# Optimization experiments

Measured on AMD Instinct MI355X. Metric: run time of the kernel, lower is better.

The kernel has to match this reference:

```python
import jax, jax.numpy as jnp
import numpy as np

D_MODEL = 1024
D_STATE = 16
D_CONV = 4
EXPAND = 2
D_INNER = EXPAND * D_MODEL          # 2048
DT_RANK = D_MODEL // 16             # 64 (ceil(d_model/16))
B, L = 2, 2048


def setup_inputs() -> dict:
    key = jax.random.key(0)
    ks = jax.random.split(key, 8)
    s = 0.02
    return {
        "x": jax.random.normal(ks[0], (B, L, D_MODEL), jnp.float32),
        "ln_w": jnp.ones((D_MODEL,), jnp.float32),
        "ln_b": jnp.zeros((D_MODEL,), jnp.float32),
        "W_in": jax.random.normal(ks[1], (2 * D_INNER, D_MODEL), jnp.float32) * s,
        "conv_w": jax.random.normal(ks[2], (D_INNER, 1, D_CONV), jnp.float32) * s,
        "conv_b": jnp.zeros((D_INNER,), jnp.float32),
        "W_xproj": jax.random.normal(ks[3], (DT_RANK + 2 * D_STATE, D_INNER), jnp.float32) * s,
        "W_dt": jax.random.normal(ks[4], (D_INNER, DT_RANK), jnp.float32) * s,
        "b_dt": jax.random.normal(ks[5], (D_INNER,), jnp.float32) * 0.1,
        "A_log": jnp.log(jnp.broadcast_to(
            jnp.arange(1, D_STATE + 1, dtype=jnp.float32), (D_INNER, D_STATE))),
        "D_skip": jnp.ones((D_INNER,), jnp.float32),
        "W_out": jax.random.normal(ks[6], (D_MODEL, D_INNER), jnp.float32) * s,
    }


def reference(x, ln_w, ln_b, W_in, conv_w, conv_b, W_xproj, W_dt, b_dt,
              A_log, D_skip, W_out):
    # --- LayerNorm ---
    mu = jnp.mean(x, -1, keepdims=True)
    var = jnp.var(x, -1, keepdims=True)
    xn = (x - mu) * jax.lax.rsqrt(var + 1e-5) * ln_w + ln_b

    # --- in_proj -> (x_ssm, z gate) ---
    xz = jnp.einsum('bld,ed->ble', xn, W_in)          # [B,L,2*D_INNER]
    xs, z = jnp.split(xz, 2, axis=-1)                 # each [B,L,D_INNER]

    # --- depthwise causal conv1d + SiLU ---
    xc = jnp.transpose(xs, (0, 2, 1))                 # [B,D_INNER,L]
    xc = jax.lax.conv_general_dilated(
        xc, conv_w, window_strides=(1,), padding=[(D_CONV - 1, 0)],
        dimension_numbers=('NCH', 'OIH', 'NCH'),
        feature_group_count=D_INNER)
    xc = xc + conv_b[None, :, None]
    xs = jax.nn.silu(jnp.transpose(xc, (0, 2, 1)))    # [B,L,D_INNER]

    # --- input-dependent SSM params ---
    x_dbl = jnp.einsum('bld,ed->ble', xs, W_xproj)    # [B,L,DT_RANK+2*D_STATE]
    dt, Bm, Cm = jnp.split(x_dbl, [DT_RANK, DT_RANK + D_STATE], axis=-1)
    dt = jax.nn.softplus(jnp.einsum('blr,dr->bld', dt, W_dt) + b_dt)  # [B,L,D_INNER]

    A = -jnp.exp(A_log)                               # [D_INNER,D_STATE]
    deltaA = jnp.exp(dt[..., None] * A)               # [B,L,D_INNER,D_STATE]
    deltaBx = dt[..., None] * Bm[:, :, None, :] * xs[..., None]

    # --- selective scan over time ---
    def step(h, inp):
        dA, dBx, C = inp                              # [B,Din,S],[B,Din,S],[B,S]
        h = dA * h + dBx
        y = jnp.einsum('bds,bs->bd', h, C)
        return h, y

    h0 = jnp.zeros((x.shape[0], D_INNER, D_STATE), xs.dtype)
    _, ys = jax.lax.scan(step, h0, (jnp.moveaxis(deltaA, 1, 0),
                                    jnp.moveaxis(deltaBx, 1, 0),
                                    jnp.moveaxis(Cm, 1, 0)))
    y = jnp.moveaxis(ys, 0, 1) + xs * D_skip          # [B,L,D_INNER]

    # --- gate + out_proj + residual ---
    y = y * jax.nn.silu(z)
    out = jnp.einsum('bld,ed->ble', y, W_out)         # [B,L,D_MODEL]
    return x + out
```

## Files before the change

kernel.cpp:

```cpp
#include <hip/hip_runtime.h>
#include <hip/hip_bf16.h>


typedef __attribute__((ext_vector_type(4))) float f32x4;
typedef __attribute__((ext_vector_type(8))) short s16x8;

static __device__ __forceinline__ float b2f(ushort u) {
  union { float f; unsigned int i; } v; v.i = ((unsigned int)u) << 16; return v.f;
}
static __device__ __forceinline__ ushort f2b(float f) {
  union { __hip_bfloat16 h; ushort u; } v; v.h = __float2bfloat16(f); return v.u;
}

#define GLD16(gp, lp) __builtin_amdgcn_global_load_lds( \
    (const __attribute__((address_space(1))) void*)(gp), \
    (__attribute__((address_space(3))) void*)(lp), 16, 0, 0)

__global__ void prep_weights_kernel(const float* __restrict__ W_in,
    const float* __restrict__ W_out, const float* __restrict__ W_dt,
    const float* __restrict__ W_xproj, ushort* __restrict__ win,
    ushort* __restrict__ wout, ushort* __restrict__ wdt, ushort* __restrict__ wxp) {
  int i = blockIdx.x * 256 + threadIdx.x;
  if (i < 1048576) {
    float4 v = ((const float4*)W_in)[i];
    ((ushort4*)win)[i] = make_ushort4(f2b(v.x), f2b(v.y), f2b(v.z), f2b(v.w));
    return;
  }
  i -= 1048576;
  if (i < 524288) {
    float4 v = ((const float4*)W_out)[i];
    ((ushort4*)wout)[i] = make_ushort4(f2b(v.x), f2b(v.y), f2b(v.z), f2b(v.w));
    return;
  }
  i -= 524288;
  if (i < 32768) {
    float4 v = ((const float4*)W_dt)[i];
    ((ushort4*)wdt)[i] = make_ushort4(f2b(v.x), f2b(v.y), f2b(v.z), f2b(v.w));
    return;
  }
  i -= 32768;
  if (i < 65536) {
    int e  = i >> 9;
    int k4 = (i & 511) << 2;
    ushort4 o = make_ushort4(0, 0, 0, 0);
    if (e < 96) {
      float4 v = *(const float4*)(W_xproj + (size_t)e * 2048 + k4);
      o = make_ushort4(f2b(v.x), f2b(v.y), f2b(v.z), f2b(v.w));
    }
    ((ushort4*)wxp)[i] = o;
  }
}

__global__ __launch_bounds__(256) void ln_kernel(const float* __restrict__ x,
    const float* __restrict__ w, const float* __restrict__ b, ushort* __restrict__ xn) {
  const int row = blockIdx.x;
  const int tid = threadIdx.x;
  float4 v = ((const float4*)(x + (size_t)row * 1024))[tid];
  float s  = v.x + v.y + v.z + v.w;
  float s2 = v.x*v.x + v.y*v.y + v.z*v.z + v.w*v.w;
  #pragma unroll
  for (int off = 32; off; off >>= 1) { s += __shfl_xor(s, off); s2 += __shfl_xor(s2, off); }
  __shared__ float red[8];
  if ((tid & 63) == 0) { red[tid >> 6] = s; red[(tid >> 6) + 4] = s2; }
  __syncthreads();
  float S  = red[0] + red[1] + red[2] + red[3];
  float S2 = red[4] + red[5] + red[6] + red[7];
  float mu   = S * (1.0f / 1024.0f);
  float var  = S2 * (1.0f / 1024.0f) - mu * mu;
  float rstd = rsqrtf(var + 1e-5f);
  float4 wv = ((const float4*)w)[tid];
  float4 bv = ((const float4*)b)[tid];
  ushort4 o = make_ushort4(
      f2b((v.x - mu) * rstd * wv.x + bv.x),
      f2b((v.y - mu) * rstd * wv.y + bv.y),
      f2b((v.z - mu) * rstd * wv.z + bv.z),
      f2b((v.w - mu) * rstd * wv.w + bv.w));
  ((ushort4*)(xn + (size_t)row * 1024))[tid] = o;
}

template<int EPI>
__global__ __launch_bounds__(256, 2) void gemm_db(
    const ushort* __restrict__ A, const ushort* __restrict__ B,
    float* __restrict__ Cf, ushort* __restrict__ Cb,
    const float* __restrict__ aux,
    int M, int N, int K, int kt_per)
{
  __shared__ __align__(16) char SM[49152];
  const int tid  = threadIdx.x;
  const int lane = tid & 63;
  const int wid  = tid >> 6;
  const int wr = wid >> 1, wc = wid & 1;
  const int m0 = blockIdx.x * 64, n0 = blockIdx.y * 128;
  const int kt0 = blockIdx.z * kt_per;

  const int srow = tid >> 3;
  const int sxor = ((tid & 7) ^ (srow & 7)) << 3;
  const ushort* Ag = A + (size_t)(m0 + srow) * K + sxor + (size_t)kt0 * 64;
  const ushort* Bg = B + (size_t)(n0 + srow) * K + sxor + (size_t)kt0 * 64;
  const size_t rstep = (size_t)32 * K;
  char* lds0 = (char*)SM + wid * 1024;

  f32x4 acc[2][4];
  #pragma unroll
  for (int m = 0; m < 2; ++m)
    #pragma unroll
    for (int n = 0; n < 4; ++n)
      acc[m][n] = (f32x4){0.f, 0.f, 0.f, 0.f};

  const int frow = lane & 15;
  const int fk   = (lane >> 4) << 3;
  const int sw   = (lane & 7) << 3;

#define STAGE(sel, ktv) { \
    const ushort* ag = Ag + (size_t)(ktv) * 64; \
    const ushort* bg = Bg + (size_t)(ktv) * 64; \
    char* ba = lds0 + (sel) * 24576; \
    GLD16(ag,             ba); \
    GLD16(ag + rstep,     ba + 4096); \
    GLD16(bg,             ba + 8192); \
    GLD16(bg + rstep,     ba + 12288); \
    GLD16(bg + 2 * rstep, ba + 16384); \
    GLD16(bg + 3 * rstep, ba + 20480); \
  }

#define COMPUTE(sel) { \
    const ushort* Asb = (const ushort*)((const char*)SM + (sel) * 24576); \
    const ushort* Bsb = Asb + 4096;  \
    _Pragma("unroll") \
    for (int kk = 0; kk < 2; ++kk) { \
      const int col = (kk * 32 + fk) ^ sw; \
      s16x8 af[2], bf[4]; \
      _Pragma("unroll") \
      for (int m = 0; m < 2; ++m) \
        af[m] = *(const s16x8*)(Asb + (wr * 32 + m * 16 + frow) * 64 + col); \
      _Pragma("unroll") \
      for (int n = 0; n < 4; ++n) \
        bf[n] = *(const s16x8*)(Bsb + (wc * 64 + n * 16 + frow) * 64 + col); \
      _Pragma("unroll") \
      for (int m = 0; m < 2; ++m) \
        _Pragma("unroll") \
        for (int n = 0; n < 4; ++n) \
          acc[m][n] = __builtin_amdgcn_mfma_f32_16x16x32_bf16(af[m], bf[n], acc[m][n], 0, 0, 0); \
    } \
  }

  STAGE(0, 0);
  __syncthreads();
  int c = 0;
  for (int kt = 0; kt < kt_per - 1; ++kt) {
    STAGE(c ^ 1, kt + 1);
    COMPUTE(c);
    __syncthreads();
    c ^= 1;
  }
  COMPUTE(c);
  __syncthreads();

  float* epi = (float*)SM;
  const int rl = tid >> 3;
  const int c0 = (tid & 7) << 4;
  const size_t zoff = (EPI == 2) ? (size_t)blockIdx.z * M * N : 0;
  #pragma unroll
  for (int m = 0; m < 2; ++m) {
    #pragma unroll
    for (int n = 0; n < 4; ++n) {
      const int cl = wc * 64 + n * 16 + (lane & 15);
      #pragma unroll
      for (int j = 0; j < 4; ++j) {
        const int rr = wr * 16 + ((lane >> 4) << 2) + j;
        epi[rr * 132 + cl] = acc[m][n][j];
      }
    }
    __syncthreads();
    const int grow = m0 + ((rl >> 4) << 5) + m * 16 + (rl & 15);
    const int gcol = n0 + c0;
    float v[16];
    #pragma unroll
    for (int q = 0; q < 16; ++q) v[q] = epi[rl * 132 + c0 + q];
    if (EPI == 1) {
      ushort u[16];
      #pragma unroll
      for (int q = 0; q < 16; ++q) u[q] = f2b(v[q]);
      *(int4*)(Cb + (size_t)grow * N + gcol)     = *(int4*)&u[0];
      *(int4*)(Cb + (size_t)grow * N + gcol + 8) = *(int4*)&u[8];
    } else if (EPI == 2) {
      #pragma unroll
      for (int q = 0; q < 4; ++q)
        *(float4*)(Cf + zoff + (size_t)grow * N + gcol + q * 4) = *(float4*)&v[q * 4];
    } else if (EPI == 3) {
      ushort u[16];
      #pragma unroll
      for (int q = 0; q < 4; ++q) {
        float4 bb = *(const float4*)(aux + gcol + q * 4);
        float t0 = v[q*4+0] + bb.x, t1 = v[q*4+1] + bb.y;
        float t2 = v[q*4+2] + bb.z, t3 = v[q*4+3] + bb.w;
        u[q*4+0] = f2b(fmaxf(t0, 0.f) + __logf(1.f + __expf(-fabsf(t0))));
        u[q*4+1] = f2b(fmaxf(t1, 0.f) + __logf(1.f + __expf(-fabsf(t1))));
        u[q*4+2] = f2b(fmaxf(t2, 0.f) + __logf(1.f + __expf(-fabsf(t2))));
        u[q*4+3] = f2b(fmaxf(t3, 0.f) + __logf(1.f + __expf(-fabsf(t3))));
      }
      *(int4*)(Cb + (size_t)grow * N + gcol)     = *(int4*)&u[0];
      *(int4*)(Cb + (size_t)grow * N + gcol + 8) = *(int4*)&u[8];
    } else {
      #pragma unroll
      for (int q = 0; q < 4; ++q) {
        float4 rr2 = *(const float4*)(aux + (size_t)grow * N + gcol + q * 4);
        float4 ov = make_float4(rr2.x + v[q*4+0], rr2.y + v[q*4+1],
                                rr2.z + v[q*4+2], rr2.w + v[q*4+3]);
        *(float4*)(Cf + (size_t)grow * N + gcol + q * 4) = ov;
      }
    }
    __syncthreads();
  }
#undef STAGE
#undef COMPUTE
}

__global__ __launch_bounds__(256) void conv_silu_kernel(const ushort* __restrict__ xz,
    const float* __restrict__ cw, const float* __restrict__ cb, ushort* __restrict__ xs) {
  const int idx = blockIdx.x * 256 + threadIdx.x;
  const int d4 = idx & 511;
  const int lg = (idx >> 9) & 511;
  const int b  = idx >> 18;
  const int d  = d4 << 2;
  const int l0 = lg << 2;
  float w[4][4];
  const float* cwd = cw + d * 4;
  #pragma unroll
  for (int j = 0; j < 4; ++j)
    #pragma unroll
    for (int t = 0; t < 4; ++t) w[j][t] = cwd[j * 4 + t];
  const float4 bias = *(const float4*)(cb + d);
  float vin[7][4];
  const size_t base = (size_t)(b * 2048) * 4096 + d;
  #pragma unroll
  for (int j = 0; j < 7; ++j) {
    const int ls = l0 - 3 + j;
    if (ls >= 0) {
      ushort4 xv = *(const ushort4*)(xz + base + (size_t)ls * 4096);
      vin[j][0] = b2f(xv.x); vin[j][1] = b2f(xv.y);
      vin[j][2] = b2f(xv.z); vin[j][3] = b2f(xv.w);
    } else {
      vin[j][0] = vin[j][1] = vin[j][2] = vin[j][3] = 0.f;
    }
  }
  #pragma unroll
  for (int i = 0; i < 4; ++i) {
    float a0 = bias.x, a1 = bias.y, a2 = bias.z, a3 = bias.w;
    #pragma unroll
    for (int t = 0; t < 4; ++t) {
      a0 += vin[i + t][0] * w[0][t];
      a1 += vin[i + t][1] * w[1][t];
      a2 += vin[i + t][2] * w[2][t];
      a3 += vin[i + t][3] * w[3][t];
    }
    ushort4 o;
    o.x = f2b(a0 / (1.f + __expf(-a0)));
    o.y = f2b(a1 / (1.f + __expf(-a1)));
    o.z = f2b(a2 / (1.f + __expf(-a2)));
    o.w = f2b(a3 / (1.f + __expf(-a3)));
    *(ushort4*)(xs + (size_t)(b * 2048 + l0 + i) * 2048 + d) = o;
  }
}

__global__ __launch_bounds__(256) void xdbl_reduce_kernel(const float* __restrict__ x8,
    float* __restrict__ xdbl, ushort* __restrict__ dtlow) {
  const int i = blockIdx.x * 256 + threadIdx.x;
  const int r = i >> 5, c4 = (i & 31) << 2;
  float4 s = make_float4(0.f, 0.f, 0.f, 0.f);
  #pragma unroll
  for (int z = 0; z < 8; ++z) {
    float4 v = *(const float4*)(x8 + (size_t)z * 524288 + (size_t)r * 128 + c4);
    s.x += v.x; s.y += v.y; s.z += v.z; s.w += v.w;
  }
  *(float4*)(xdbl + (size_t)r * 128 + c4) = s;
  if (c4 < 64) {
    ((ushort4*)(dtlow + (size_t)r * 64))[c4 >> 2] =
        make_ushort4(f2b(s.x), f2b(s.y), f2b(s.z), f2b(s.w));
  }
}

__global__ __launch_bounds__(256, 4) void scanA_kernel(const ushort* __restrict__ dt,
    const ushort* __restrict__ xs, const float* __restrict__ xdbl,
    const float* __restrict__ A_log, float* __restrict__ FH, float* __restrict__ Sdt) {
  __shared__ float Bsh[32 * 16];
  const int tid = threadIdx.x;
  const int d = blockIdx.x * 256 + tid;
  const int c = blockIdx.y, b = blockIdx.z;
  const int t0 = b * 2048 + c * 32;
  if (tid < 128) {
    const int il = tid >> 2, q = (tid & 3) << 2;
    *(float4*)&Bsh[il * 16 + q] = *(const float4*)(xdbl + (size_t)(t0 + il) * 128 + 64 + q);
  }
  float Ad[16];
  #pragma unroll
  for (int s = 0; s < 16; ++s) Ad[s] = -__expf(A_log[(size_t)d * 16 + s]);
  __syncthreads();
  float h[16];
  #pragma unroll
  for (int s = 0; s < 16; ++s) h[s] = 0.f;
  float sdt = 0.f;
  const ushort* dtp = dt + (size_t)t0 * 2048 + d;
  const ushort* xsp = xs + (size_t)t0 * 2048 + d;
  float dtv = b2f(dtp[0]);
  float xv  = b2f(xsp[0]);
  for (int il = 0; il < 32; ++il) {
    float dtn = 0.f, xn = 0.f;
    if (il < 31) { dtn = b2f(dtp[(il + 1) * 2048]); xn = b2f(xsp[(il + 1) * 2048]); }
    const float dx = dtv * xv;
    sdt += dtv;
    const float* Bv = &Bsh[il * 16];
    #pragma unroll
    for (int s = 0; s < 16; ++s) h[s] = __expf(dtv * Ad[s]) * h[s] + dx * Bv[s];
    dtv = dtn; xv = xn;
  }
  const size_t fo = (((size_t)b * 64 + c) * 2048 + d) * 16;
  #pragma unroll
  for (int q = 0; q < 4; ++q)
    *(float4*)(FH + fo + q * 4) = make_float4(h[q*4], h[q*4+1], h[q*4+2], h[q*4+3]);
  Sdt[((size_t)b * 64 + c) * 2048 + d] = sdt;
}

__global__ __launch_bounds__(256) void scanB_kernel(float* __restrict__ FH,
    const float* __restrict__ Sdt, const float* __restrict__ A_log) {
  const int idx = blockIdx.x * 256 + threadIdx.x;
  const int s = idx & 15;
  const int d = (idx >> 4) & 2047;
  const int b = idx >> 15;
  const float Ad = -__expf(A_log[(size_t)d * 16 + s]);
  float H = 0.f;
  #pragma unroll 8
  for (int c = 0; c < 64; ++c) {
    const size_t o = (((size_t)b * 64 + c) * 2048 + d) * 16 + s;
    const float F   = FH[o];
    const float sdt = Sdt[((size_t)b * 64 + c) * 2048 + d];
    FH[o] = H;
    H = __expf(sdt * Ad) * H + F;
  }
}

__global__ __launch_bounds__(256, 4) void scanC_kernel(const ushort* __restrict__ dt,
    const ushort* __restrict__ xs, const float* __restrict__ xdbl,
    const ushort* __restrict__ xz, const float* __restrict__ A_log,
    const float* __restrict__ Dskip, const float* __restrict__ FH,
    ushort* __restrict__ yg) {
  __shared__ float BCsh[32 * 32];
  const int tid = threadIdx.x;
  const int d = blockIdx.x * 256 + tid;
  const int c = blockIdx.y, b = blockIdx.z;
  const int t0 = b * 2048 + c * 32;
  {
    const int il = tid >> 3, q = (tid & 7) << 2;
    *(float4*)&BCsh[il * 32 + q] = *(const float4*)(xdbl + (size_t)(t0 + il) * 128 + 64 + q);
  }
  float Ad[16];
  #pragma unroll
  for (int s = 0; s < 16; ++s) Ad[s] = -__expf(A_log[(size_t)d * 16 + s]);
  float h[16];
  const size_t ho = (((size_t)b * 64 + c) * 2048 + d) * 16;
  {
    const float4* Hp = (const float4*)(FH + ho);
    float4 H0 = Hp[0], H1 = Hp[1], H2 = Hp[2], H3 = Hp[3];
    h[0]=H0.x; h[1]=H0.y; h[2]=H0.z; h[3]=H0.w;
    h[4]=H1.x; h[5]=H1.y; h[6]=H1.z; h[7]=H1.w;
    h[8]=H2.x; h[9]=H2.y; h[10]=H2.z; h[11]=H2.w;
    h[12]=H3.x; h[13]=H3.y; h[14]=H3.z; h[15]=H3.w;
  }
  __syncthreads();
  const float Dk = Dskip[d];
  const ushort* dtp = dt + (size_t)t0 * 2048 + d;
  const ushort* xsp = xs + (size_t)t0 * 2048 + d;
  const ushort* zp  = xz + (size_t)t0 * 4096 + 2048 + d;
  ushort* ygp = yg + (size_t)t0 * 2048 + d;
  float dtv = b2f(dtp[0]);
  float xv  = b2f(xsp[0]);
  float zv  = b2f(zp[0]);
  for (int il = 0; il < 32; ++il) {
    float dtn = 0.f, xn = 0.f, zn = 0.f;
    if (il < 31) {
      dtn = b2f(dtp[(il + 1) * 2048]);
      xn  = b2f(xsp[(il + 1) * 2048]);
      zn  = b2f(zp[(size_t)(il + 1) * 4096]);
    }
    const float dx = dtv * xv;
    const float* Bv = &BCsh[il * 32];
    const float* Cv = &BCsh[il * 32 + 16];
    float y = 0.f;
    #pragma unroll
    for (int s = 0; s < 16; ++s) {
      h[s] = __expf(dtv * Ad[s]) * h[s] + dx * Bv[s];
      y += h[s] * Cv[s];
    }
    const float g = zv / (1.f + __expf(-zv));
    ygp[il * 2048] = f2b((y + xv * Dk) * g);
    dtv = dtn; xv = xn; zv = zn;
  }
}

extern "C" void kernel_launch(void* const* d_in, const int* in_sizes, int n_in,
                              void* d_out, int out_size, void* d_ws, size_t ws_size,
                              hipStream_t stream) {
  (void)in_sizes; (void)n_in; (void)out_size; (void)ws_size;
  const float* x       = (const float*)d_in[0];
  const float* ln_w    = (const float*)d_in[1];
  const float* ln_b    = (const float*)d_in[2];
  const float* W_in    = (const float*)d_in[3];
  const float* conv_w  = (const float*)d_in[4];
  const float* conv_b  = (const float*)d_in[5];
  const float* W_xproj = (const float*)d_in[6];
  const float* W_dt    = (const float*)d_in[7];
  const float* b_dt    = (const float*)d_in[8];
  const float* A_log   = (const float*)d_in[9];
  const float* D_skip  = (const float*)d_in[10];
  const float* W_out   = (const float*)d_in[11];
  float* out = (float*)d_out;

  char* ws = (char*)d_ws;
  size_t off = 0;
  auto alloc = [&](size_t bytes) -> void* {
    void* p = ws + off;
    off += (bytes + 255) & ~(size_t)255;
    return p;
  };
  ushort* win_bf   = (ushort*)alloc((size_t)4096 * 1024 * 2);
  ushort* wout_bf  = (ushort*)alloc((size_t)1024 * 2048 * 2);
  ushort* wxp_bf   = (ushort*)alloc((size_t)128 * 2048 * 2);
  ushort* wdt_bf   = (ushort*)alloc((size_t)2048 * 64 * 2);
  ushort* xn_bf    = (ushort*)alloc((size_t)4096 * 1024 * 2);
  ushort* xz_bf    = (ushort*)alloc((size_t)4096 * 4096 * 2);
  ushort* xs_bf    = (ushort*)alloc((size_t)4096 * 2048 * 2);
  float*  xdbl     = (float*)alloc((size_t)4096 * 128 * 4);
  float*  xdbl8    = (float*)alloc((size_t)8 * 4096 * 128 * 4);
  ushort* dtlow_bf = (ushort*)alloc((size_t)4096 * 64 * 2);
  ushort* dtf_bf   = (ushort*)alloc((size_t)4096 * 2048 * 2);
  float*  SdtBuf   = (float*)alloc((size_t)2 * 64 * 2048 * 4);
  ushort* yg_bf    = (ushort*)alloc((size_t)4096 * 2048 * 2);
  float*  FH       = xdbl8;

  prep_weights_kernel<<<6528, 256, 0, stream>>>(W_in, W_out, W_dt, W_xproj,
                                                win_bf, wout_bf, wdt_bf, wxp_bf);
  ln_kernel<<<4096, 256, 0, stream>>>(x, ln_w, ln_b, xn_bf);

  gemm_db<1><<<dim3(64, 32, 1), 256, 0, stream>>>(xn_bf, win_bf, nullptr, xz_bf,
                                                  nullptr, 4096, 4096, 1024, 16);
  conv_silu_kernel<<<2048, 256, 0, stream>>>(xz_bf, conv_w, conv_b, xs_bf);

  gemm_db<2><<<dim3(64, 1, 8), 256, 0, stream>>>(xs_bf, wxp_bf, xdbl8, nullptr,
                                                 nullptr, 4096, 128, 2048, 4);
  xdbl_reduce_kernel<<<512, 256, 0, stream>>>(xdbl8, xdbl, dtlow_bf);

  gemm_db<3><<<dim3(64, 16, 1), 256, 0, stream>>>(dtlow_bf, wdt_bf, nullptr, dtf_bf,
                                                  b_dt, 4096, 2048, 64, 1);

  scanA_kernel<<<dim3(8, 64, 2), 256, 0, stream>>>(dtf_bf, xs_bf, xdbl, A_log, FH, SdtBuf);
  scanB_kernel<<<256, 256, 0, stream>>>(FH, SdtBuf, A_log);
  scanC_kernel<<<dim3(8, 64, 2), 256, 0, stream>>>(dtf_bf, xs_bf, xdbl, xz_bf, A_log, D_skip,
                                                   FH, yg_bf);

  gemm_db<4><<<dim3(64, 8, 1), 256, 0, stream>>>(yg_bf, wout_bf, out, nullptr, x,
                                                 4096, 1024, 2048, 32);
}
```

Before: 290.7 us.

## Add 128x128-tile bf16 MFMA GEMM for the in_proj matmul

Adds a new gemm_big kernel with 128x128 output tiles, a K-step of 32 and 4x4 MFMA fragments per wave, and uses it for the 4096x4096x1024 in_proj GEMM instead of the 64x128 double-buffered kernel. The larger tile raises arithmetic intensity per LDS/global load and halves the block count. The cost is twice as many K iterations, each with its own barrier, and LDS reads without the XOR swizzle, which may cause bank conflicts. The EPI==1 path is removed from the old kernel.

```diff
diff --git a/kernel.cpp b/kernel.cpp
--- a/kernel.cpp
+++ b/kernel.cpp
@@ -79,6 +79,105 @@
 }
 
 template<int EPI>
+__global__ __launch_bounds__(256, 3) void gemm_big(
+    const ushort* __restrict__ A, const ushort* __restrict__ B,
+    float* __restrict__ Cf, ushort* __restrict__ Cb,
+    const float* __restrict__ aux,
+    int M, int N, int K, int kt_per)
+{
+  __shared__ __align__(16) char SM[33024];
+  const int tid  = threadIdx.x;
+  const int lane = tid & 63;
+  const int wid  = tid >> 6;
+  const int wr = wid >> 1, wc = wid & 1;
+  const int m0 = blockIdx.x * 128, n0 = blockIdx.y * 128;
+  const int nt = kt_per;
+
+  const int srow = tid >> 2;
+  const int scol = (tid & 3) << 3;
+  const ushort* Ag = A + (size_t)(m0 + srow) * K + scol;
+  const ushort* Bg = B + (size_t)(n0 + srow) * K + scol;
+  const size_t rstep = (size_t)64 * K;
+  char* lds0 = (char*)SM + wid * 1024;
+
+  f32x4 acc[4][4];
+  #pragma unroll
+  for (int m = 0; m < 4; ++m)
+    #pragma unroll
+    for (int n = 0; n < 4; ++n)
+      acc[m][n] = (f32x4){0.f, 0.f, 0.f, 0.f};
+
+  const int frow = lane & 15;
+  const int fk   = (lane >> 4) << 3;
+
+#define BSTAGE(sel, ktv) { \
+    const size_t ko = (size_t)(ktv) * 32; \
+    char* ba = lds0 + (sel) * 16384; \
+    GLD16(Ag + ko,         ba); \
+    GLD16(Ag + ko + rstep, ba + 4096); \
+    GLD16(Bg + ko,         ba + 8192); \
+    GLD16(Bg + ko + rstep, ba + 12288); \
+  }
+
+#define BCOMPUTE(sel) { \
+    const ushort* Asb = (const ushort*)((const char*)SM + (sel) * 16384); \
+    const ushort* Bsb = Asb + 4096;  \
+    s16x8 af[4], bf[4]; \
+    _Pragma("unroll") \
+    for (int m = 0; m < 4; ++m) \
+      af[m] = *(const s16x8*)(Asb + (wr * 64 + m * 16 + frow) * 32 + fk); \
+    _Pragma("unroll") \
+    for (int n = 0; n < 4; ++n) \
+      bf[n] = *(const s16x8*)(Bsb + (wc * 64 + n * 16 + frow) * 32 + fk); \
+    _Pragma("unroll") \
+    for (int m = 0; m < 4; ++m) \
+      _Pragma("unroll") \
+      for (int n = 0; n < 4; ++n) \
+        acc[m][n] = __builtin_amdgcn_mfma_f32_16x16x32_bf16(af[m], bf[n], acc[m][n], 0, 0, 0); \
+  }
+
+  BSTAGE(0, 0);
+  __syncthreads();
+  for (int t = 0; t < nt; ++t) {
+    if (t + 1 < nt) BSTAGE((t + 1) & 1, t + 1);
+    BCOMPUTE(t & 1);
+    __syncthreads();
+  }
+
+  float* epi = (float*)SM;
+  const int rl = tid >> 3;
+  const int c0 = (tid & 7) << 4;
+  #pragma unroll
+  for (int m = 0; m < 4; ++m) {
+    #pragma unroll
+    for (int n = 0; n < 4; ++n) {
+      const int cl = wc * 64 + n * 16 + (lane & 15);
+      #pragma unroll
+      for (int j = 0; j < 4; ++j) {
+        const int rr = wr * 16 + ((lane >> 4) << 2) + j;
+        epi[rr * 132 + cl] = acc[m][n][j];
+      }
+    }
+    __syncthreads();
+    const int grow = m0 + ((rl >> 4) << 6) + m * 16 + (rl & 15);
+    const int gcol = n0 + c0;
+    float v[16];
+    #pragma unroll
+    for (int q = 0; q < 16; ++q) v[q] = epi[rl * 132 + c0 + q];
+    if (EPI == 1) {
+      ushort u[16];
+      #pragma unroll
+      for (int q = 0; q < 16; ++q) u[q] = f2b(v[q]);
+      *(int4*)(Cb + (size_t)grow * N + gcol)     = *(int4*)&u[0];
+      *(int4*)(Cb + (size_t)grow * N + gcol + 8) = *(int4*)&u[8];
+    }
+    __syncthreads();
+  }
+#undef BSTAGE
+#undef BCOMPUTE
+}
+
+template<int EPI>
 __global__ __launch_bounds__(256, 2) void gemm_db(
     const ushort* __restrict__ A, const ushort* __restrict__ B,
     float* __restrict__ Cf, ushort* __restrict__ Cb,
@@ -125,7 +224,7 @@
 
 #define COMPUTE(sel) { \
     const ushort* Asb = (const ushort*)((const char*)SM + (sel) * 24576); \
-    const ushort* Bsb = Asb + 4096;  \
+    const ushort* Bsb = Asb + 4096; \
     _Pragma("unroll") \
     for (int kk = 0; kk < 2; ++kk) { \
       const int col = (kk * 32 + fk) ^ sw; \
@@ -177,13 +276,7 @@
     float v[16];
     #pragma unroll
     for (int q = 0; q < 16; ++q) v[q] = epi[rl * 132 + c0 + q];
-    if (EPI == 1) {
-      ushort u[16];
-      #pragma unroll
-      for (int q = 0; q < 16; ++q) u[q] = f2b(v[q]);
-      *(int4*)(Cb + (size_t)grow * N + gcol)     = *(int4*)&u[0];
-      *(int4*)(Cb + (size_t)grow * N + gcol + 8) = *(int4*)&u[8];
-    } else if (EPI == 2) {
+    if (EPI == 2) {
       #pragma unroll
       for (int q = 0; q < 4; ++q)
         *(float4*)(Cf + zoff + (size_t)grow * N + gcol + q * 4) = *(float4*)&v[q * 4];
@@ -441,8 +534,8 @@
                                                 win_bf, wout_bf, wdt_bf, wxp_bf);
   ln_kernel<<<4096, 256, 0, stream>>>(x, ln_w, ln_b, xn_bf);
 
-  gemm_db<1><<<dim3(64, 32, 1), 256, 0, stream>>>(xn_bf, win_bf, nullptr, xz_bf,
-                                                  nullptr, 4096, 4096, 1024, 16);
+  gemm_big<1><<<dim3(32, 32, 1), 256, 0, stream>>>(xn_bf, win_bf, nullptr, xz_bf,
+                                                   nullptr, 4096, 4096, 1024, 32);
   conv_silu_kernel<<<2048, 256, 0, stream>>>(xz_bf, conv_w, conv_b, xs_bf);
 
   gemm_db<2><<<dim3(64, 1, 8), 256, 0, stream>>>(xs_bf, wxp_bf, xdbl8, nullptr,
```

After: 289.4 us. Within noise of the previous version (-0.5%).
